# Optimization experiments

Measured on AMD Instinct MI355X. Metric: run time of the kernel, lower is better.

The kernel has to match this reference:

```python
import jax, jax.numpy as jnp
import numpy as np
import math

N_USR = 50000
N_ENT = 100000
D = 64
N_REL = 16
E = 1_000_000
EI = 500_000
N_HEADS = 2


def setup_inputs() -> dict:
    key = jax.random.key(0)
    ks = jax.random.split(key, 9)
    user_emb = jax.random.normal(ks[0], (N_USR, D), jnp.float32) * 0.1
    entity_emb = jax.random.normal(ks[1], (N_ENT, D), jnp.float32) * 0.1
    edge_index = jax.random.randint(ks[2], (2, E), 0, N_ENT, dtype=jnp.int32)
    edge_type = jax.random.randint(ks[3], (E,), 1, N_REL + 1, dtype=jnp.int32)  # values in [1, N_REL]
    inter_u = jax.random.randint(ks[4], (EI,), 0, N_USR, dtype=jnp.int32)
    inter_i = jax.random.randint(ks[5], (EI,), 0, N_ENT, dtype=jnp.int32)
    inter_edge = jnp.stack([inter_u, inter_i], axis=0)
    inter_edge_w = jax.random.uniform(ks[6], (EI,), jnp.float32)
    relation_emb = jax.random.normal(ks[7], (N_REL, D), jnp.float32) * 0.1
    W_Q = jax.random.normal(ks[8], (D, D), jnp.float32) * 0.1
    return {
        'layers_num': 2,
        'user_emb': user_emb,
        'entity_emb': entity_emb,
        'inter_edge': inter_edge,
        'inter_edge_w': inter_edge_w,
        'edge_index': edge_index,
        'edge_type': edge_type,
        'relation_emb': relation_emb,
        'W_Q': W_Q,
    }


def _scatter_softmax(scores, idx, n_segments):
    # scores: [E, H]; softmax over edges sharing the same head index
    m = jax.ops.segment_max(scores, idx, num_segments=n_segments)  # [n, H]
    ex = jnp.exp(scores - m[idx])
    denom = jax.ops.segment_sum(ex, idx, num_segments=n_segments)
    return ex / denom[idx]


def reference(layers_num, user_emb, entity_emb, inter_edge, inter_edge_w, edge_index, edge_type, relation_emb, W_Q):
    n_entities = entity_emb.shape[0]
    n_users = user_emb.shape[0]
    d = entity_emb.shape[1]
    h = N_HEADS
    dk = d // h
    head, tail = edge_index[0], edge_index[1]
    iu, ii = inter_edge[0], inter_edge[1]

    def agg_layer(u_emb, e_emb):
        rel = relation_emb[edge_type - 1]                                # [E, d]
        query = (e_emb[head] @ W_Q).reshape(-1, h, dk)                   # [E, h, dk]
        key = (e_emb[tail] @ W_Q).reshape(-1, h, dk) * rel.reshape(-1, h, dk)
        score = (query * key).sum(-1) / math.sqrt(dk)                    # [E, h]
        attn = _scatter_softmax(score, head, n_entities)                 # [E, h]
        value = (e_emb[tail] * rel).reshape(-1, h, dk)                   # [E, h, dk]
        entity_agg = (value * attn[:, :, None]).reshape(-1, d)           # [E, d]
        entity_agg = jax.ops.segment_sum(entity_agg, head, num_segments=n_entities)
        # F.normalize (L2, eps=1e-12)
        norm = jnp.sqrt(jnp.sum(entity_agg * entity_agg, axis=1, keepdims=True))
        entity_agg = entity_agg / jnp.maximum(norm, 1e-12)
        item_agg = inter_edge_w[:, None] * e_emb[ii]                      # [Ei, d]
        user_agg = jax.ops.segment_sum(item_agg, iu, num_segments=n_users)
        return entity_agg, user_agg

    user_embs = [user_emb]
    entity_embs = [entity_emb]
    u, e = user_emb, entity_emb
    for _ in range(layers_num):
        e, u = agg_layer(u, e)
        user_embs.append(u)
        entity_embs.append(e)
    user_out = jnp.mean(jnp.stack(user_embs, axis=1), axis=1)
    entity_out = jnp.mean(jnp.stack(entity_embs, axis=1), axis=1)
    return (user_out, entity_out)
```

## Files before the change

### kernel.cpp

```cpp
#include <hip/hip_runtime.h>
#include <hip/hip_fp16.h>
#include <math.h>

#define N_USR 50000
#define N_ENT 100000
#define DIM   64
#define NE    1000000
#define NEI   500000

#define BKW   125
#define EBK   800
#define UBK   400
#define CAP   1664
#define KCH   4096
#define NBA_E 245
#define NBA_U 123

#define NBE_B 12500
#define NBU_B 6250

__device__ __forceinline__ __half2 pick_lo(unsigned a, unsigned b) {
    unsigned r = __builtin_amdgcn_perm(b, a, 0x05040100u);
    return *(__half2*)&r;
}
__device__ __forceinline__ __half2 pick_hi(unsigned a, unsigned b) {
    unsigned r = __builtin_amdgcn_perm(b, a, 0x07060302u);
    return *(__half2*)&r;
}

template <int CTRL>
__device__ __forceinline__ float dpp_add(float x) {
    int y = __builtin_amdgcn_update_dpp(0, __builtin_bit_cast(int, x),
                                        CTRL, 0xF, 0xF, true);
    return x + __builtin_bit_cast(float, y);
}

__device__ __forceinline__ int swz16_maxi(int x) {
    int t = __builtin_amdgcn_ds_swizzle(x, 0x401F);
    return max(x, t);
}

typedef _Float16 fp16x2 __attribute__((ext_vector_type(2)));
__device__ __forceinline__ float dot2(__half2 a, __half2 b, float c) {
#if __has_builtin(__builtin_amdgcn_fdot2)
    return __builtin_amdgcn_fdot2(__builtin_bit_cast(fp16x2, a),
                                  __builtin_bit_cast(fp16x2, b), c, false);
#else
    __half2 m = __hmul2(a, b);
    return c + __low2float(m) + __high2float(m);
#endif
}

__device__ __forceinline__ float exp2_fast(float x) {
#if __has_builtin(__builtin_amdgcn_exp2f)
    return __builtin_amdgcn_exp2f(x);
#else
    return exp2f(x);
#endif
}

__global__ __launch_bounds__(256) void k_gemm(const float* __restrict__ Emat,
                                              const float* __restrict__ WQ,
                                              unsigned int* __restrict__ Gu,
                                              __half* __restrict__ Eh, int nrows) {
    int lane = threadIdx.x & 63;
    int wid  = (int)((blockIdx.x * 256 + threadIdx.x) >> 6);
    int nw   = (int)((gridDim.x * 256) >> 6);
    float w[64];
#pragma unroll
    for (int k = 0; k < 64; k++) w[k] = WQ[k * 64 + lane];
    for (int row = wid; row < nrows; row += nw) {
        int rowu = __builtin_amdgcn_readfirstlane(row);
        const float* er = Emat + (size_t)rowu * DIM;
        float acc = 0.f;
#pragma unroll
        for (int k = 0; k < 64; k++) acc = fmaf(er[k], w[k], acc);
        float ecol = er[lane];
        unsigned short hp = __half_as_ushort(__float2half(acc));
        unsigned short he = __half_as_ushort(__float2half(ecol));
        Gu[(size_t)rowu * 64 + lane] = (unsigned int)hp | ((unsigned int)he << 16);
        Eh[(size_t)rowu * 64 + lane] = __ushort_as_half(he);
    }
}

__global__ __launch_bounds__(256) void k_bucketA(const int* __restrict__ eidx,
                                                 const int* __restrict__ etype,
                                                 const int* __restrict__ inter,
                                                 const float* __restrict__ w,
                                                 int* __restrict__ gcnt,
                                                 int* __restrict__ ebuf,
                                                 int2* __restrict__ ubuf) {
    __shared__ int ch[EBK];
    int tid = threadIdx.x;
    int blk = blockIdx.x;
    for (int j = tid; j < EBK; j += 256) ch[j] = 0;
    __syncthreads();
    if (blk < NBA_E) {
        int lo = blk * KCH, hi = min(lo + KCH, NE);
        for (int i = lo + tid; i < hi; i += 256)
            atomicAdd(&ch[eidx[i] / BKW], 1);
        __syncthreads();
        for (int j = tid; j < EBK; j += 256)
            ch[j] = atomicAdd(&gcnt[j], ch[j]);
        __syncthreads();
        for (int i = lo + tid; i < hi; i += 256) {
            int head = eidx[i];
            int b    = head / BKW;
            int pos  = atomicAdd(&ch[b], 1);
            if (pos < CAP)
                ebuf[b * CAP + pos] = eidx[NE + i] | ((etype[i] - 1) << 20)
                                      | ((head - b * BKW) << 24);
        }
    } else {
        int ub = blk - NBA_E;
        int lo = ub * KCH, hi = min(lo + KCH, NEI);
        for (int i = lo + tid; i < hi; i += 256)
            atomicAdd(&ch[inter[i] / BKW], 1);
        __syncthreads();
        for (int j = tid; j < UBK; j += 256)
            ch[j] = atomicAdd(&gcnt[EBK + j], ch[j]);
        __syncthreads();
        for (int i = lo + tid; i < hi; i += 256) {
            int u   = inter[i];
            int b   = u / BKW;
            int pos = atomicAdd(&ch[b], 1);
            if (pos < CAP)
                ubuf[b * CAP + pos] = make_int2(inter[NEI + i] | ((u - b * BKW) << 24),
                                                __float_as_int(w[i]));
        }
    }
}

__global__ __launch_bounds__(512) void k_bucketB(const int* __restrict__ gcnt,
                                                 const int* __restrict__ ebuf,
                                                 const int2* __restrict__ ubuf,
                                                 int2* __restrict__ off2_e,
                                                 int* __restrict__ edges,
                                                 int2* __restrict__ off2_u,
                                                 int2* __restrict__ iw) {
    __shared__ int h[512];
    __shared__ int cur[512];
    __shared__ int s0[CAP];
    __shared__ int s1[CAP];
    int tid = threadIdx.x;
    int b   = blockIdx.x;
    bool isU = (b >= EBK);
    int lb   = isU ? b - EBK : b;
    int n    = min(gcnt[b], CAP);
    int base = lb * BKW;
    int gbase = lb * CAP;
    h[tid] = 0;
    __syncthreads();
    if (!isU) {
        const int* src = ebuf + (size_t)lb * CAP;
        for (int q = tid; q < n; q += 512) atomicAdd(&h[((unsigned)src[q]) >> 24], 1);
        __syncthreads();
        int v = h[tid];
        for (int d = 1; d < 512; d <<= 1) {
            int x = (tid >= d) ? h[tid - d] : 0;
            __syncthreads();
            h[tid] += x;
            __syncthreads();
        }
        int excl = h[tid] - v;
        cur[tid] = excl;
        if (tid < BKW) off2_e[base + tid] = make_int2(gbase + excl, v);
        __syncthreads();
        for (int q = tid; q < n; q += 512) {
            int x = src[q];
            int r = atomicAdd(&cur[((unsigned)x) >> 24], 1);
            s0[r] = x;
        }
        __syncthreads();
        for (int q = tid; q < n; q += 512) edges[gbase + q] = s0[q] & 0xFFFFFF;
    } else {
        const int2* src = ubuf + (size_t)lb * CAP;
        for (int q = tid; q < n; q += 512) atomicAdd(&h[((unsigned)src[q].x) >> 24], 1);
        __syncthreads();
        int v = h[tid];
        for (int d = 1; d < 512; d <<= 1) {
            int x = (tid >= d) ? h[tid - d] : 0;
            __syncthreads();
            h[tid] += x;
            __syncthreads();
        }
        int excl = h[tid] - v;
        cur[tid] = excl;
        if (tid < BKW) off2_u[base + tid] = make_int2(gbase + excl, v);
        __syncthreads();
        for (int q = tid; q < n; q += 512) {
            int2 x = src[q];
            int r = atomicAdd(&cur[((unsigned)x.x) >> 24], 1);
            s0[r] = x.x;
            s1[r] = x.y;
        }
        __syncthreads();
        for (int q = tid; q < n; q += 512)
            iw[gbase + q] = make_int2(s0[q] & 0xFFFFFF, s1[q]);
    }
}

#define ENT_GATHER(G, R, PK)                                                  \
    {                                                                         \
        G = *(const uint4*)(Gu + (size_t)(unsigned)(PK & 0xFFFFF) * 64 + 4 * dq); \
        R = *(const uint2*)(srel2 + ((((unsigned)PK >> 20) << 5) + dq2));     \
    }

#define ENT_BODY(G, R, KK)                                                    \
    {                                                                         \
        __half2 ra = *(__half2*)&(R).x;                                       \
        __half2 rb = *(__half2*)&(R).y;                                       \
        float sc = dot2(q2a, __hmul2(pick_lo((G).x, (G).y), ra), 0.f);        \
        sc = dot2(q2b, __hmul2(pick_lo((G).z, (G).w), rb), sc);               \
        sc = dpp_add<0xB1>(sc);                                               \
        sc = dpp_add<0x4E>(sc);                                               \
        sc = dpp_add<0x141>(sc);                                              \
        float ex = ((KK) < deg) ? exp2_fast(sc) : 0.f;                        \
        den += ex;                                                            \
        __half2 va = __hmul2(pick_hi((G).x, (G).y), ra);                      \
        __half2 vb = __hmul2(pick_hi((G).z, (G).w), rb);                      \
        acc0 = fmaf(ex, __low2float(va), acc0);                               \
        acc1 = fmaf(ex, __high2float(va), acc1);                              \
        acc2 = fmaf(ex, __low2float(vb), acc2);                               \
        acc3 = fmaf(ex, __high2float(vb), acc3);                              \
    }

__device__ __forceinline__ void ent_path(const unsigned int* __restrict__ Gu,
                                         const unsigned int* srel2,
                                         const int2* __restrict__ off2,
                                         const int* __restrict__ edges,
                                         float* __restrict__ enext,
                                         float* __restrict__ out_ent,
                                         const float* __restrict__ base0,
                                         int mode, int row0, int lane) {
    int grp  = lane >> 4;
    int dq   = lane & 15;
    int dq2  = 2 * dq;
    int row  = row0 + grp;
    uint4 qg = *(const uint4*)(Gu + (size_t)row * 64 + 4 * dq);
    const __half2 qs = __float2half2_rn(0.17677669529663687f * 1.44269504088896340f);
    __half2 q2a = __hmul2(pick_lo(qg.x, qg.y), qs);
    __half2 q2b = __hmul2(pick_lo(qg.z, qg.w), qs);
    int2 od = off2[row];
    int lo = od.x, deg = od.y;
    int km = swz16_maxi(deg);
    km = max(km, __shfl_xor(km, 32, 64));
    float acc0 = 0.f, acc1 = 0.f, acc2 = 0.f, acc3 = 0.f, den = 0.f;
    const int* ep = edges + lo;
    int r0 = ep[0], r1 = ep[1], r2 = ep[2], r3 = ep[3];
    for (int k = 0; k < km; k += 4) {
        int e0v = r0, e1v = r1, e2v = r2, e3v = r3;
        if (k + 4 < km) {
            r0 = ep[k + 4]; r1 = ep[k + 5]; r2 = ep[k + 6]; r3 = ep[k + 7];
        }
        int p0 = (k + 0 < deg) ? e0v : 0;
        int p1 = (k + 1 < deg) ? e1v : 0;
        int p2 = (k + 2 < deg) ? e2v : 0;
        int p3 = (k + 3 < deg) ? e3v : 0;
        bool c1 = (k + 1 < km), c2 = (k + 2 < km), c3 = (k + 3 < km);
        uint4 G0, G1, G2, G3;
        uint2 R0, R1, R2, R3;
        ENT_GATHER(G0, R0, p0);
        if (c1) ENT_GATHER(G1, R1, p1);
        if (c2) ENT_GATHER(G2, R2, p2);
        if (c3) ENT_GATHER(G3, R3, p3);
        ENT_BODY(G0, R0, k);
        if (c1) ENT_BODY(G1, R1, k + 1);
        if (c2) ENT_BODY(G2, R2, k + 2);
        if (c3) ENT_BODY(G3, R3, k + 3);
    }
    float rden = (den > 0.f) ? 1.0f / den : 0.f;
    float rx = acc0 * rden, ry = acc1 * rden, rz = acc2 * rden, rw = acc3 * rden;
    float ss = rx * rx + ry * ry + rz * rz + rw * rw;
    ss = dpp_add<0xB1>(ss);
    ss = dpp_add<0x4E>(ss);
    ss = dpp_add<0x141>(ss);
    ss = dpp_add<0x140>(ss);
    float inv = 1.0f / fmaxf(sqrtf(ss), 1e-12f);
    size_t idx = (size_t)row * 16 + dq;
    float4 y = make_float4(rx * inv, ry * inv, rz * inv, rw * inv);
    if (mode == 0) {
        ((float4*)enext)[idx] = y;
        float4 b0 = ((const float4*)base0)[idx];
        ((float4*)out_ent)[idx] = make_float4(b0.x + y.x, b0.y + y.y,
                                              b0.z + y.z, b0.w + y.w);
    } else {
        float4 o = ((float4*)out_ent)[idx];
        ((float4*)out_ent)[idx] = make_float4((o.x + y.x) * (1.0f / 3.0f),
                                              (o.y + y.y) * (1.0f / 3.0f),
                                              (o.z + y.z) * (1.0f / 3.0f),
                                              (o.w + y.w) * (1.0f / 3.0f));
    }
}

#define USR_BODY(G, WV, KK)                                                   \
    {                                                                         \
        float cw = ((KK) < deg) ? (WV) : 0.f;                                 \
        __half2 h0 = *(__half2*)&(G).x;                                       \
        __half2 h1 = *(__half2*)&(G).y;                                       \
        acc0 = fmaf(cw, __low2float(h0), acc0);                               \
        acc1 = fmaf(cw, __high2float(h0), acc1);                              \
        acc2 = fmaf(cw, __low2float(h1), acc2);                               \
        acc3 = fmaf(cw, __high2float(h1), acc3);                              \
    }

__device__ __forceinline__ void usr_path(const unsigned int* __restrict__ Eh2,
                                         const int2* __restrict__ off2,
                                         const int2* __restrict__ iw,
                                         float* __restrict__ out_user,
                                         const float* __restrict__ base0,
                                         int mode, int row0, int lane) {
    int grp  = lane >> 4;
    int dq   = lane & 15;
    int dq2  = 2 * dq;
    int row  = row0 + grp;
    int2 od = off2[row];
    int lo = od.x, deg = od.y;
    int km = swz16_maxi(deg);
    km = max(km, __shfl_xor(km, 32, 64));
    float acc0 = 0.f, acc1 = 0.f, acc2 = 0.f, acc3 = 0.f;
    const int2* vp = iw + lo;
    int2 v0 = vp[0], v1 = vp[1], v2 = vp[2], v3 = vp[3];
    for (int k = 0; k < km; k += 4) {
        int2 u0 = v0, u1 = v1, u2 = v2, u3 = v3;
        if (k + 4 < km) {
            v0 = vp[k + 4]; v1 = vp[k + 5]; v2 = vp[k + 6]; v3 = vp[k + 7];
        }
        int t0 = (k + 0 < deg) ? u0.x : 0;
        int t1 = (k + 1 < deg) ? u1.x : 0;
        int t2 = (k + 2 < deg) ? u2.x : 0;
        int t3 = (k + 3 < deg) ? u3.x : 0;
        bool c1 = (k + 1 < km), c2 = (k + 2 < km), c3 = (k + 3 < km);
        uint2 g0, g1, g2, g3;
        g0 = *(const uint2*)(Eh2 + (size_t)t0 * 32 + dq2);
        if (c1) g1 = *(const uint2*)(Eh2 + (size_t)t1 * 32 + dq2);
        if (c2) g2 = *(const uint2*)(Eh2 + (size_t)t2 * 32 + dq2);
        if (c3) g3 = *(const uint2*)(Eh2 + (size_t)t3 * 32 + dq2);
        USR_BODY(g0, __int_as_float(u0.y), k);
        if (c1) USR_BODY(g1, __int_as_float(u1.y), k + 1);
        if (c2) USR_BODY(g2, __int_as_float(u2.y), k + 2);
        if (c3) USR_BODY(g3, __int_as_float(u3.y), k + 3);
    }
    size_t idx = (size_t)row * 16 + dq;
    if (mode == 0) {
        float4 b0 = ((const float4*)base0)[idx];
        ((float4*)out_user)[idx] = make_float4(b0.x + acc0, b0.y + acc1,
                                               b0.z + acc2, b0.w + acc3);
    } else {
        float4 o = ((float4*)out_user)[idx];
        ((float4*)out_user)[idx] = make_float4((o.x + acc0) * (1.0f / 3.0f),
                                               (o.y + acc1) * (1.0f / 3.0f),
                                               (o.z + acc2) * (1.0f / 3.0f),
                                               (o.w + acc3) * (1.0f / 3.0f));
    }
}

__global__ __launch_bounds__(128) void k_agg(const unsigned int* __restrict__ Gu,
                                             const unsigned int* __restrict__ Eh2,
                                             const float* __restrict__ rel,
                                             const int2* __restrict__ off2_e,
                                             const int* __restrict__ edges,
                                             const int2* __restrict__ off2_u,
                                             const int2* __restrict__ iw,
                                             float* __restrict__ enext,
                                             float* __restrict__ out_ent,
                                             const float* __restrict__ ent0,
                                             float* __restrict__ out_user,
                                             const float* __restrict__ usr0,
                                             int mode) {
    __shared__ unsigned int srel2[16 * 32];
    int tid = threadIdx.x;
    int b   = blockIdx.x;
    int g   = b / 3;
    int r   = b - 3 * g;
    int lane = tid & 63;
    int wv   = tid >> 6;
    if (r < 2) {
        for (int i = tid; i < 16 * 32; i += 128) {
            float2 rp = ((const float2*)rel)[i];
            __half2 h = __floats2half2_rn(rp.x, rp.y);
            srel2[i] = *(unsigned int*)&h;
        }
        __syncthreads();
        int row0 = (2 * g + r) * 8 + wv * 4;
        ent_path(Gu, srel2, off2_e, edges, enext, out_ent, ent0, mode, row0, lane);
    } else {
        int row0 = g * 8 + wv * 4;
        usr_path(Eh2, off2_u, iw, out_user, usr0, mode, row0, lane);
    }
}

extern "C" void kernel_launch(void* const* d_in, const int* in_sizes, int n_in,
                              void* d_out, int out_size, void* d_ws, size_t ws_size,
                              hipStream_t stream) {
    const float* user_emb   = (const float*)d_in[1];
    const float* entity_emb = (const float*)d_in[2];
    const int*   inter_edge = (const int*)d_in[3];
    const float* inter_w    = (const float*)d_in[4];
    const int*   edge_index = (const int*)d_in[5];
    const int*   edge_type  = (const int*)d_in[6];
    const float* rel_emb    = (const float*)d_in[7];
    const float* wq         = (const float*)d_in[8];

    float* out      = (float*)d_out;
    float* out_user = out;
    float* out_ent  = out + (size_t)N_USR * DIM;

    const size_t SZ_E = (size_t)N_ENT * DIM * sizeof(float);
    char* ws = (char*)d_ws;
    size_t o = 0;
#define ALIGN16() o = (o + 15) & ~(size_t)15
    unsigned int* Gu = (unsigned int*)(ws + o); o += (size_t)N_ENT * 64 * 4;
    __half* Eh     = (__half*)(ws + o); o += (size_t)N_ENT * 64 * 2;
    float* eA      = (float*)(ws + o); o += SZ_E;
    ALIGN16();
    int*   edges   = (int*)  (ws + o); o += ((size_t)EBK * CAP + CAP + 16) * 4;
    ALIGN16();
    int2*  off2_e  = (int2*) (ws + o); o += (size_t)N_ENT * 8;
    ALIGN16();
    int2*  iw      = (int2*) (ws + o); o += ((size_t)UBK * CAP + CAP + 16) * 8;
    int2*  off2_u  = (int2*) (ws + o); o += (size_t)N_USR * 8;
    ALIGN16();
    int*   ebuf    = (int*)  (ws + o); o += (size_t)EBK * CAP * 4;
    ALIGN16();
    int2*  ubuf    = (int2*) (ws + o); o += (size_t)UBK * CAP * 8;
    int*   gcnt    = (int*)  (ws + o); o += (EBK + UBK) * 4;

    hipMemsetAsync(gcnt, 0, (EBK + UBK) * 4, stream);
    k_bucketA<<<NBA_E + NBA_U, 256, 0, stream>>>(edge_index, edge_type,
                                                 inter_edge, inter_w, gcnt,
                                                 ebuf, ubuf);
    k_bucketB<<<EBK + UBK, 512, 0, stream>>>(gcnt, ebuf, ubuf,
                                             off2_e, edges, off2_u, iw);

    const int layers = 2;
    for (int L = 0; L < layers; L++) {
        const float* ecur = (L == 0) ? entity_emb : eA;
        k_gemm<<<1536, 256, 0, stream>>>(ecur, wq, Gu, Eh, N_ENT);
        k_agg<<<NBE_B + NBU_B, 128, 0, stream>>>(Gu, (const unsigned int*)Eh, rel_emb,
                                                 off2_e, edges, off2_u, iw,
                                                 eA, out_ent, entity_emb,
                                                 out_user, user_emb, L);
    }
}
```

Baseline: 306.5 us.

## Use MFMA for entity projection and drop separate half entity buffer

Measured after the change: 296.0 us. -3.4%, faster.

```diff
diff --git a/kernel.cpp b/kernel.cpp
--- a/kernel.cpp
+++ b/kernel.cpp
@@ -41,6 +41,9 @@
 }
 
 typedef _Float16 fp16x2 __attribute__((ext_vector_type(2)));
+typedef _Float16 half8 __attribute__((ext_vector_type(8)));
+typedef float floatx4 __attribute__((ext_vector_type(4)));
+
 __device__ __forceinline__ float dot2(__half2 a, __half2 b, float c) {
 #if __has_builtin(__builtin_amdgcn_fdot2)
     return __builtin_amdgcn_fdot2(__builtin_bit_cast(fp16x2, a),
@@ -62,25 +65,52 @@
 __global__ __launch_bounds__(256) void k_gemm(const float* __restrict__ Emat,
                                               const float* __restrict__ WQ,
                                               unsigned int* __restrict__ Gu,
-                                              __half* __restrict__ Eh, int nrows) {
+                                              int ntiles) {
     int lane = threadIdx.x & 63;
-    int wid  = (int)((blockIdx.x * 256 + threadIdx.x) >> 6);
-    int nw   = (int)((gridDim.x * 256) >> 6);
-    float w[64];
-#pragma unroll
-    for (int k = 0; k < 64; k++) w[k] = WQ[k * 64 + lane];
-    for (int row = wid; row < nrows; row += nw) {
-        int rowu = __builtin_amdgcn_readfirstlane(row);
-        const float* er = Emat + (size_t)rowu * DIM;
-        float acc = 0.f;
-#pragma unroll
-        for (int k = 0; k < 64; k++) acc = fmaf(er[k], w[k], acc);
-        float ecol = er[lane];
-        unsigned short hp = __half_as_ushort(__float2half(acc));
-        unsigned short he = __half_as_ushort(__float2half(ecol));
-        Gu[(size_t)rowu * 64 + lane] = (unsigned int)hp | ((unsigned int)he << 16);
-        Eh[(size_t)rowu * 64 + lane] = __ushort_as_half(he);
-    }
+    int tile = (int)((blockIdx.x * 256 + threadIdx.x) >> 6);
+    if (tile >= ntiles) return;
+    int m = lane & 15;
+    int g = lane >> 4;
+    half8 wf[2][4];
+#pragma unroll
+    for (int s = 0; s < 2; s++)
+#pragma unroll
+        for (int t = 0; t < 4; t++)
+#pragma unroll
+            for (int j = 0; j < 8; j++)
+                wf[s][t][j] = (_Float16)WQ[(s * 32 + g * 8 + j) * 64 + t * 16 + m];
+    const float* ar = Emat + (size_t)(tile * 16 + m) * 64 + g * 8;
+    float4 fa0 = *(const float4*)ar;
+    float4 fa1 = *(const float4*)(ar + 4);
+    float4 fb0 = *(const float4*)(ar + 32);
+    float4 fb1 = *(const float4*)(ar + 36);
+    half8 a0, a1;
+    a0[0] = (_Float16)fa0.x; a0[1] = (_Float16)fa0.y;
+    a0[2] = (_Float16)fa0.z; a0[3] = (_Float16)fa0.w;
+    a0[4] = (_Float16)fa1.x; a0[5] = (_Float16)fa1.y;
+    a0[6] = (_Float16)fa1.z; a0[7] = (_Float16)fa1.w;
+    a1[0] = (_Float16)fb0.x; a1[1] = (_Float16)fb0.y;
+    a1[2] = (_Float16)fb0.z; a1[3] = (_Float16)fb0.w;
+    a1[4] = (_Float16)fb1.x; a1[5] = (_Float16)fb1.y;
+    a1[6] = (_Float16)fb1.z; a1[7] = (_Float16)fb1.w;
+    floatx4 acc[4];
+#pragma unroll
+    for (int t = 0; t < 4; t++) {
+        acc[t] = (floatx4){0.f, 0.f, 0.f, 0.f};
+        acc[t] = __builtin_amdgcn_mfma_f32_16x16x32_f16(a0, wf[0][t], acc[t], 0, 0, 0);
+        acc[t] = __builtin_amdgcn_mfma_f32_16x16x32_f16(a1, wf[1][t], acc[t], 0, 0, 0);
+    }
+#pragma unroll
+    for (int t = 0; t < 4; t++)
+#pragma unroll
+        for (int r = 0; r < 4; r++) {
+            int row = tile * 16 + g * 4 + r;
+            int col = t * 16 + m;
+            float e = Emat[(size_t)row * 64 + col];
+            unsigned short hp = __half_as_ushort(__float2half(acc[t][r]));
+            unsigned short he = __half_as_ushort(__float2half(e));
+            Gu[(size_t)row * 64 + col] = (unsigned)hp | ((unsigned)he << 16);
+        }
 }
 
 __global__ __launch_bounds__(256) void k_bucketA(const int* __restrict__ eidx,
@@ -296,15 +326,15 @@
 #define USR_BODY(G, WV, KK)                                                   \
     {                                                                         \
         float cw = ((KK) < deg) ? (WV) : 0.f;                                 \
-        __half2 h0 = *(__half2*)&(G).x;                                       \
-        __half2 h1 = *(__half2*)&(G).y;                                       \
+        __half2 h0 = pick_hi((G).x, (G).y);                                   \
+        __half2 h1 = pick_hi((G).z, (G).w);                                   \
         acc0 = fmaf(cw, __low2float(h0), acc0);                               \
         acc1 = fmaf(cw, __high2float(h0), acc1);                              \
         acc2 = fmaf(cw, __low2float(h1), acc2);                               \
         acc3 = fmaf(cw, __high2float(h1), acc3);                              \
     }
 
-__device__ __forceinline__ void usr_path(const unsigned int* __restrict__ Eh2,
+__device__ __forceinline__ void usr_path(const unsigned int* __restrict__ Gu,
                                          const int2* __restrict__ off2,
                                          const int2* __restrict__ iw,
                                          float* __restrict__ out_user,
@@ -312,7 +342,6 @@
                                          int mode, int row0, int lane) {
     int grp  = lane >> 4;
     int dq   = lane & 15;
-    int dq2  = 2 * dq;
     int row  = row0 + grp;
     int2 od = off2[row];
     int lo = od.x, deg = od.y;
@@ -331,11 +360,11 @@
         int t2 = (k + 2 < deg) ? u2.x : 0;
         int t3 = (k + 3 < deg) ? u3.x : 0;
         bool c1 = (k + 1 < km), c2 = (k + 2 < km), c3 = (k + 3 < km);
-        uint2 g0, g1, g2, g3;
-        g0 = *(const uint2*)(Eh2 + (size_t)t0 * 32 + dq2);
-        if (c1) g1 = *(const uint2*)(Eh2 + (size_t)t1 * 32 + dq2);
-        if (c2) g2 = *(const uint2*)(Eh2 + (size_t)t2 * 32 + dq2);
-        if (c3) g3 = *(const uint2*)(Eh2 + (size_t)t3 * 32 + dq2);
+        uint4 g0, g1, g2, g3;
+        g0 = *(const uint4*)(Gu + (size_t)t0 * 64 + 4 * dq);
+        if (c1) g1 = *(const uint4*)(Gu + (size_t)t1 * 64 + 4 * dq);
+        if (c2) g2 = *(const uint4*)(Gu + (size_t)t2 * 64 + 4 * dq);
+        if (c3) g3 = *(const uint4*)(Gu + (size_t)t3 * 64 + 4 * dq);
         USR_BODY(g0, __int_as_float(u0.y), k);
         if (c1) USR_BODY(g1, __int_as_float(u1.y), k + 1);
         if (c2) USR_BODY(g2, __int_as_float(u2.y), k + 2);
@@ -356,7 +385,6 @@
 }
 
 __global__ __launch_bounds__(128) void k_agg(const unsigned int* __restrict__ Gu,
-                                             const unsigned int* __restrict__ Eh2,
                                              const float* __restrict__ rel,
                                              const int2* __restrict__ off2_e,
                                              const int* __restrict__ edges,
@@ -386,7 +414,7 @@
         ent_path(Gu, srel2, off2_e, edges, enext, out_ent, ent0, mode, row0, lane);
     } else {
         int row0 = g * 8 + wv * 4;
-        usr_path(Eh2, off2_u, iw, out_user, usr0, mode, row0, lane);
+        usr_path(Gu, off2_u, iw, out_user, usr0, mode, row0, lane);
     }
 }
 
@@ -411,7 +439,6 @@
     size_t o = 0;
 #define ALIGN16() o = (o + 15) & ~(size_t)15
     unsigned int* Gu = (unsigned int*)(ws + o); o += (size_t)N_ENT * 64 * 4;
-    __half* Eh     = (__half*)(ws + o); o += (size_t)N_ENT * 64 * 2;
     float* eA      = (float*)(ws + o); o += SZ_E;
     ALIGN16();
     int*   edges   = (int*)  (ws + o); o += ((size_t)EBK * CAP + CAP + 16) * 4;
@@ -434,10 +461,11 @@
                                              off2_e, edges, off2_u, iw);
 
     const int layers = 2;
+    const int ntiles = N_ENT / 16;
     for (int L = 0; L < layers; L++) {
         const float* ecur = (L == 0) ? entity_emb : eA;
-        k_gemm<<<1536, 256, 0, stream>>>(ecur, wq, Gu, Eh, N_ENT);
-        k_agg<<<NBE_B + NBU_B, 128, 0, stream>>>(Gu, (const unsigned int*)Eh, rel_emb,
+        k_gemm<<<(ntiles + 3) / 4, 256, 0, stream>>>(ecur, wq, Gu, ntiles);
+        k_agg<<<NBE_B + NBU_B, 128, 0, stream>>>(Gu, rel_emb,
                                                  off2_e, edges, off2_u, iw,
                                                  eA, out_ent, entity_emb,
                                                  out_user, user_emb, L);
```
